# Performance work log

Hardware: AMD Instinct MI355X
Metric: run time of the kernel (lower is better)

The kernel has to match this reference:

```python
import jax, jax.numpy as jnp
import numpy as np

TEMPERATURE = 0.1
NUM_RISK_GROUPS = 4
SIM_WEIGHT = 1.0
CONTRAST_WEIGHT = 0.1
NEG = jnp.float32(-1e9)  # finite stand-in for -inf (grad-safe, exp() == 0 in fp32)


def setup_inputs() -> dict:
    key = jax.random.key(0)
    k1, k2, k3, k4 = jax.random.split(key, 4)
    N, D = 8192, 256
    return {
        "log_risks": jax.random.normal(k1, (N,), dtype=jnp.float32),
        "times": jax.random.uniform(k2, (N,), dtype=jnp.float32),
        "censor": jnp.ones((N,), dtype=jnp.int32),
        "wsi_embeddings": jax.random.normal(k3, (N, D), dtype=jnp.float32),
        "omic_embeddings": jax.random.normal(k4, (N, D), dtype=jnp.float32),
    }


def _cox_loss(log_risks, times, censor):
    lr = jnp.clip(log_risks, -10.0, 10.0)
    order = jnp.argsort(-times)  # descending times
    slr = lr[order]
    sc = censor[order]
    # at-risk sum for index i is sum_{j<=i} exp(slr_j) (arange <= i mask) -> cumsum
    at_risk = jnp.cumsum(jnp.exp(slr))
    li = slr - jnp.log(at_risk + 1e-15)
    mask = (sc == 1)
    cnt = jnp.maximum(jnp.sum(mask), 1)
    return -jnp.sum(jnp.where(mask, li, 0.0)) / cnt


def _similarity_loss(a, b):
    na = jnp.maximum(jnp.linalg.norm(a, axis=1), 1e-8)
    nb = jnp.maximum(jnp.linalg.norm(b, axis=1), 1e-8)
    cos = jnp.clip(jnp.sum(a * b, axis=1) / (na * nb), -1.0, 1.0)
    return jnp.mean(1.0 - cos)


def _contrastive_loss(emb, times):
    # NOTE: assumes censor == 1 for all samples (as in setup_inputs), so the
    # uncensored subset is the whole batch and shapes stay static.
    G = NUM_RISK_GROUPS
    q = jnp.quantile(times, jnp.linspace(0.0, 1.0, G + 1))
    # group = #thresholds q[1..G] that t >= ; max bucket clipped to G-1
    groups = jnp.clip(jnp.sum(times[:, None] >= q[None, 1:], axis=1), 0, G - 1)
    z = emb / jnp.maximum(jnp.linalg.norm(emb, axis=1, keepdims=True), 1e-12)
    sim = (z @ z.T) / TEMPERATURE  # [N, N]
    N = emb.shape[0]
    eye = jnp.eye(N, dtype=bool)
    same = groups[:, None] == groups[None, :]
    pos = same & ~eye
    offdiag = ~eye  # pos | neg == all off-diagonal entries
    lse_pos = jax.nn.logsumexp(jnp.where(pos, sim, NEG), axis=1)
    lse_all = jax.nn.logsumexp(jnp.where(offdiag, sim, NEG), axis=1)
    neg_any = jnp.any(~same & ~eye, axis=1)
    valid = jnp.any(pos, axis=1) & neg_any
    loss = -lse_pos + lse_all
    cnt = jnp.maximum(jnp.sum(valid), 1)
    return jnp.sum(jnp.where(valid, loss, 0.0)) / cnt


def reference(log_risks, times, censor, wsi_embeddings, omic_embeddings):
    cox = _cox_loss(log_risks, times, censor)
    sim = _similarity_loss(wsi_embeddings, omic_embeddings)
    c_wsi = _contrastive_loss(wsi_embeddings, times)
    c_omic = _contrastive_loss(omic_embeddings, times)
    contrast = (c_wsi + c_omic) / 2.0
    return cox + SIM_WEIGHT * sim + CONTRAST_WEIGHT * contrast
```

## Files before the change

### kernel.cpp

```cpp
#include <hip/hip_runtime.h>


#define NN 8192
#define DD 256

typedef __attribute__((ext_vector_type(4))) float f32x4;
typedef __attribute__((ext_vector_type(4))) int i32x4;
typedef __attribute__((ext_vector_type(8))) int i32x8;

__device__ inline void gl_lds16(const void* g, void* l) {
  __builtin_amdgcn_global_load_lds(
      (const __attribute__((address_space(1))) unsigned int*)g,
      (__attribute__((address_space(3))) unsigned int*)l, 16, 0, 0);
}

__global__ void __launch_bounds__(256) k_rows(
    const float* __restrict__ lr, const float* __restrict__ times,
    const int* __restrict__ censor,
    const float* __restrict__ wsi, const float* __restrict__ omic,
    unsigned char* __restrict__ pw, unsigned char* __restrict__ po,
    float* __restrict__ pslots, float* __restrict__ gsum) {
  __shared__ __align__(16) float st[1024];
  __shared__ __align__(16) float se[1024];
  __shared__ float red[4][3];
  const int tid = threadIdx.x;
  const int lane = tid & 63;
  const int wv = tid >> 6;
  const int i = blockIdx.x * 4 + wv;

  if (blockIdx.x < 64) {
    ((f32x4*)gsum)[blockIdx.x * 256 + tid] = (f32x4){0.f, 0.f, 0.f, 0.f};
  }

  const float4 w = ((const float4*)(wsi + (size_t)i * DD))[lane];
  const float4 o = ((const float4*)(omic + (size_t)i * DD))[lane];
  float nw = w.x * w.x + w.y * w.y + w.z * w.z + w.w * w.w;
  float no = o.x * o.x + o.y * o.y + o.z * o.z + o.w * o.w;
  float dd = w.x * o.x + w.y * o.y + w.z * o.z + w.w * o.w;
  for (int m = 1; m < 64; m <<= 1) {
    nw += __shfl_xor(nw, m);
    no += __shfl_xor(no, m);
    dd += __shfl_xor(dd, m);
  }
  const float nws = sqrtf(nw), nos = sqrtf(no);

  const float ti = times[i];
  int rk = 0;
  float ar = 0.f;
  for (int c = 0; c < 8; ++c) {
    __syncthreads();
    for (int p = tid; p < 1024; p += 256) {
      float t = times[c * 1024 + p];
      float l = lr[c * 1024 + p];
      st[p] = t;
      se[p] = __expf(fminf(fmaxf(l, -10.f), 10.f));
    }
    __syncthreads();
#pragma unroll 4
    for (int jt = 0; jt < 16; ++jt) {
      const int p = jt * 64 + lane;
      const float t = st[p];
      const float e = se[p];
      const bool c1 = (t < ti) || ((t == ti) && ((c * 1024 + p) < i));
      rk += c1 ? 1 : 0;
      ar += c1 ? 0.f : e;
    }
  }
  for (int m = 1; m < 64; m <<= 1) {
    rk += __shfl_xor(rk, m);
    ar += __shfl_xor(ar, m);
  }

  if (lane == 0) {
    float c = dd / (fmaxf(nws, 1e-8f) * fmaxf(nos, 1e-8f));
    c = fminf(fmaxf(c, -1.f), 1.f);
    float l = fminf(fmaxf(lr[i], -10.f), 10.f);
    float li = l - logf(ar + 1e-15f);
    bool cen = (censor[i] == 1);
    red[wv][0] = cen ? li : 0.f;
    red[wv][1] = cen ? 1.f : 0.f;
    red[wv][2] = 1.f - c;
  }

  const int r = rk;
  const float iw = 1.f / fmaxf(nws, 1e-12f);
  const float io = 1.f / fmaxf(nos, 1e-12f);
  int zw = __builtin_amdgcn_cvt_pk_fp8_f32(w.x * iw, w.y * iw, 0, false);
  zw = __builtin_amdgcn_cvt_pk_fp8_f32(w.z * iw, w.w * iw, zw, true);
  int zo = __builtin_amdgcn_cvt_pk_fp8_f32(o.x * io, o.y * io, 0, false);
  zo = __builtin_amdgcn_cvt_pk_fp8_f32(o.z * io, o.w * io, zo, true);
  const size_t off = ((size_t)((lane >> 5) * 4 + ((lane >> 3) & 3)) * NN + r) * 32
                     + (lane & 7) * 4;
  *(unsigned int*)(pw + off) = (unsigned int)zw;
  *(unsigned int*)(po + off) = (unsigned int)zo;
  __syncthreads();
  if (tid < 3) {
    pslots[blockIdx.x * 4 + tid] =
        red[0][tid] + red[1][tid] + red[2][tid] + red[3][tid];
  }
}

__global__ void __launch_bounds__(256, 4) k_contrast(
    const unsigned char* __restrict__ pw, const unsigned char* __restrict__ po,
    float* __restrict__ gsum) {
  __shared__ __align__(16) unsigned char sbuf[2][16384];
  const int tid = threadIdx.x;
  const int lane = tid & 63;
  const int wv = tid >> 6;
  const int lo = lane & 15, q = lane >> 4;
  const int cb = blockIdx.x, rb = blockIdx.y, mz = blockIdx.z;
  const unsigned char* __restrict__ pk = (mz == 0) ? pw : po;
  const int rowbase = rb * 128 + wv * 32;
  const int colstart = cb * 512;
  const int g = cb >> 2;

  i32x8 afrag[2][2];
#pragma unroll
  for (int rt = 0; rt < 2; ++rt) {
    const size_t row = rowbase + rt * 16 + lo;
#pragma unroll
    for (int ks = 0; ks < 2; ++ks)
      afrag[rt][ks] = *(const i32x8*)(pk + ((size_t)(ks * 4 + q) * NN + row) * 32);
  }

  const unsigned char* gsrc[4];
#pragma unroll
  for (int p = 0; p < 4; ++p) {
    const int u = (wv * 4 + p) * 64 + lane;
    const int uct = u >> 8, uks = (u >> 7) & 1, uh = (u >> 6) & 1;
    const int ul = u & 63;
    gsrc[p] = pk + ((size_t)(uks * 4 + (ul >> 4)) * NN
                    + colstart + uct * 16 + (ul & 15)) * 32 + uh * 16;
  }
  unsigned char* const ldb = &sbuf[0][(size_t)wv * 4096];

#pragma unroll
  for (int p = 0; p < 4; ++p) gl_lds16(gsrc[p], ldb + p * 1024);
  __syncthreads();

  float s[2][4] = {{0.f}};
  const int dctbase = (wv & 1) * 2;

#pragma unroll 1
  for (int st = 0; st < 8; ++st) {
    if (st < 7) {
      const size_t adv = (size_t)(st + 1) * 2048;
      const size_t bofs = ((st + 1) & 1) ? 16384 : 0;
#pragma unroll
      for (int p = 0; p < 4; ++p) gl_lds16(gsrc[p] + adv, ldb + bofs + p * 1024);
    }
    const unsigned char* buf = &sbuf[st & 1][0];
    const bool diagw = ((rowbase >> 6) == ((colstart + st * 64) >> 6));
#pragma unroll
    for (int ct = 0; ct < 4; ++ct) {
      f32x4 a0 = {0.f, 0.f, 0.f, 0.f}, a1 = {0.f, 0.f, 0.f, 0.f};
#pragma unroll
      for (int ks = 0; ks < 2; ++ks) {
        const int rbase = ((ct * 2 + ks) * 2) * 1024 + lane * 16;
        i32x4 blo = *(const i32x4*)&buf[rbase];
        i32x4 bhi = *(const i32x4*)&buf[rbase + 1024];
        i32x8 b = __builtin_shufflevector(blo, bhi, 0, 1, 2, 3, 4, 5, 6, 7);
        a0 = __builtin_amdgcn_mfma_scale_f32_16x16x128_f8f6f4(
            afrag[0][ks], b, a0, 0, 0, 0, 0x7F, 0, 0x7F);
        a1 = __builtin_amdgcn_mfma_scale_f32_16x16x128_f8f6f4(
            afrag[1][ks], b, a1, 0, 0, 0, 0x7F, 0, 0x7F);
      }
      if (diagw) {
#pragma unroll
        for (int r = 0; r < 4; ++r) {
          float e0 = __builtin_amdgcn_exp2f(fmaf(a0[r], 14.4269504f, -14.4269504f));
          float e1 = __builtin_amdgcn_exp2f(fmaf(a1[r], 14.4269504f, -14.4269504f));
          if (ct == dctbase + 0 && lo == q * 4 + r) e0 = 0.f;
          if (ct == dctbase + 1 && lo == q * 4 + r) e1 = 0.f;
          s[0][r] += e0;
          s[1][r] += e1;
        }
      } else {
#pragma unroll
        for (int r = 0; r < 4; ++r) {
          s[0][r] += __builtin_amdgcn_exp2f(fmaf(a0[r], 14.4269504f, -14.4269504f));
          s[1][r] += __builtin_amdgcn_exp2f(fmaf(a1[r], 14.4269504f, -14.4269504f));
        }
      }
    }
    __syncthreads();
  }

#pragma unroll
  for (int rt = 0; rt < 2; ++rt)
#pragma unroll
    for (int r = 0; r < 4; ++r) {
      float v = s[rt][r];
      v += __shfl_xor(v, 1); v += __shfl_xor(v, 2);
      v += __shfl_xor(v, 4); v += __shfl_xor(v, 8);
      if (lo == 0) {
        const int row = rowbase + rt * 16 + q * 4 + r;
        atomicAdd(&gsum[((size_t)mz * NN + row) * 4 + g], v);
      }
    }
}

__global__ void __launch_bounds__(1024) k_finale(
    const float* __restrict__ pslots, const float* __restrict__ gsum,
    float* __restrict__ out) {
  __shared__ float rsum[16][4];
  const int tid = threadIdx.x;
  const int lane = tid & 63, wv = tid >> 6;
  float cox = 0.f, cnt = 0.f, sim = 0.f, con = 0.f;
  for (int b = tid; b < 2048; b += 1024) {
    const float4 v = ((const float4*)pslots)[b];
    cox += v.x; cnt += v.y; sim += v.z;
  }
  for (int idx = tid; idx < 2 * NN; idx += 1024) {
    const float4 v = ((const float4*)gsum)[idx];
    const int row = idx & (NN - 1);
    const int gg = row >> 11;
    const float sg = (gg == 0) ? v.x : (gg == 1) ? v.y : (gg == 2) ? v.z : v.w;
    con += logf(v.x + v.y + v.z + v.w) - logf(sg);
  }
  for (int m = 1; m < 64; m <<= 1) {
    cox += __shfl_xor(cox, m);
    cnt += __shfl_xor(cnt, m);
    sim += __shfl_xor(sim, m);
    con += __shfl_xor(con, m);
  }
  if (lane == 0) {
    rsum[wv][0] = cox; rsum[wv][1] = cnt; rsum[wv][2] = sim; rsum[wv][3] = con;
  }
  __syncthreads();
  if (tid == 0) {
    float c0 = 0.f, c1 = 0.f, c2 = 0.f, c3 = 0.f;
    for (int k = 0; k < 16; ++k) {
      c0 += rsum[k][0]; c1 += rsum[k][1]; c2 += rsum[k][2]; c3 += rsum[k][3];
    }
    out[0] = -c0 / fmaxf(c1, 1.f) + c2 / (float)NN
             + 0.1f * 0.5f * c3 / (float)NN;
  }
}

extern "C" void kernel_launch(void* const* d_in, const int* in_sizes, int n_in,
                              void* d_out, int out_size, void* d_ws, size_t ws_size,
                              hipStream_t stream) {
  const float* lr = (const float*)d_in[0];
  const float* times = (const float*)d_in[1];
  const int* censor = (const int*)d_in[2];
  const float* wsi = (const float*)d_in[3];
  const float* omic = (const float*)d_in[4];
  float* out = (float*)d_out;

  char* ws = (char*)d_ws;
  float* pslots = (float*)ws;
  float* gsum = (float*)(ws + 32768);
  unsigned char* pw = (unsigned char*)(ws + 294912);
  unsigned char* po = (unsigned char*)(ws + 294912 + 2097152);

  k_rows<<<2048, 256, 0, stream>>>(lr, times, censor, wsi, omic, pw, po, pslots, gsum);
  k_contrast<<<dim3(16, 64, 2), 256, 0, stream>>>(pw, po, gsum);
  k_finale<<<1, 1024, 0, stream>>>(pslots, gsum, out);
}
```

Baseline: 149.1 us.

## Exploit similarity symmetry with triangular tiles and batch four rows per wave

The contrastive kernel now launches only the upper-triangular block tiles of the symmetric N×N similarity matrix. Off-diagonal tiles also accumulate column sums into the per-group totals through atomics, which roughly halves the MFMA and exp work. The temperature/log2 scale is folded into the fp8-normalised embeddings, and the max-offset subtraction is dropped. The rows kernel handles four rows per wave with vectorised LDS reads, amortising the O(N) rank and at-risk scan; the cost is many extra column atomics and a larger score range fed to exp2.

```diff
diff --git a/kernel.cpp b/kernel.cpp
--- a/kernel.cpp
+++ b/kernel.cpp
@@ -3,6 +3,7 @@
 
 #define NN 8192
 #define DD 256
+#define SCL 3.7982826f
 
 typedef __attribute__((ext_vector_type(4))) float f32x4;
 typedef __attribute__((ext_vector_type(4))) int i32x4;
@@ -26,73 +27,102 @@
   const int tid = threadIdx.x;
   const int lane = tid & 63;
   const int wv = tid >> 6;
-  const int i = blockIdx.x * 4 + wv;
+  const int i0 = blockIdx.x * 16 + wv * 4;
 
   if (blockIdx.x < 64) {
     ((f32x4*)gsum)[blockIdx.x * 256 + tid] = (f32x4){0.f, 0.f, 0.f, 0.f};
   }
 
-  const float4 w = ((const float4*)(wsi + (size_t)i * DD))[lane];
-  const float4 o = ((const float4*)(omic + (size_t)i * DD))[lane];
-  float nw = w.x * w.x + w.y * w.y + w.z * w.z + w.w * w.w;
-  float no = o.x * o.x + o.y * o.y + o.z * o.z + o.w * o.w;
-  float dd = w.x * o.x + w.y * o.y + w.z * o.z + w.w * o.w;
-  for (int m = 1; m < 64; m <<= 1) {
-    nw += __shfl_xor(nw, m);
-    no += __shfl_xor(no, m);
-    dd += __shfl_xor(dd, m);
-  }
-  const float nws = sqrtf(nw), nos = sqrtf(no);
-
-  const float ti = times[i];
-  int rk = 0;
-  float ar = 0.f;
+  float ti[4];
+#pragma unroll
+  for (int rr = 0; rr < 4; ++rr) ti[rr] = times[i0 + rr];
+
+  int rk[4] = {0, 0, 0, 0};
+  float ar[4] = {0.f, 0.f, 0.f, 0.f};
   for (int c = 0; c < 8; ++c) {
     __syncthreads();
-    for (int p = tid; p < 1024; p += 256) {
-      float t = times[c * 1024 + p];
-      float l = lr[c * 1024 + p];
-      st[p] = t;
-      se[p] = __expf(fminf(fmaxf(l, -10.f), 10.f));
+    {
+      const float4 t4 = ((const float4*)(times + c * 1024))[tid];
+      const float4 l4 = ((const float4*)(lr + c * 1024))[tid];
+      ((float4*)st)[tid] = t4;
+      float4 e4;
+      e4.x = __expf(fminf(fmaxf(l4.x, -10.f), 10.f));
+      e4.y = __expf(fminf(fmaxf(l4.y, -10.f), 10.f));
+      e4.z = __expf(fminf(fmaxf(l4.z, -10.f), 10.f));
+      e4.w = __expf(fminf(fmaxf(l4.w, -10.f), 10.f));
+      ((float4*)se)[tid] = e4;
     }
     __syncthreads();
-#pragma unroll 4
-    for (int jt = 0; jt < 16; ++jt) {
+#pragma unroll
+    for (int jt = 0; jt < 4; ++jt) {
       const int p = jt * 64 + lane;
-      const float t = st[p];
-      const float e = se[p];
-      const bool c1 = (t < ti) || ((t == ti) && ((c * 1024 + p) < i));
-      rk += c1 ? 1 : 0;
-      ar += c1 ? 0.f : e;
-    }
-  }
+      const float4 t = ((const float4*)st)[p];
+      const float4 e = ((const float4*)se)[p];
+      const int jb = c * 1024 + p * 4;
+#define UPD(TV, EV, JJ)                                                  \
+  {                                                                      \
+    _Pragma("unroll") for (int rr = 0; rr < 4; ++rr) {                   \
+      const bool c1 = ((TV) < ti[rr]) ||                                 \
+                      (((TV) == ti[rr]) && ((JJ) < i0 + rr));            \
+      rk[rr] += c1 ? 1 : 0;                                              \
+      ar[rr] += c1 ? 0.f : (EV);                                         \
+    }                                                                    \
+  }
+      UPD(t.x, e.x, jb + 0)
+      UPD(t.y, e.y, jb + 1)
+      UPD(t.z, e.z, jb + 2)
+      UPD(t.w, e.w, jb + 3)
+#undef UPD
+    }
+  }
+#pragma unroll
   for (int m = 1; m < 64; m <<= 1) {
-    rk += __shfl_xor(rk, m);
-    ar += __shfl_xor(ar, m);
-  }
-
+#pragma unroll
+    for (int rr = 0; rr < 4; ++rr) {
+      rk[rr] += __shfl_xor(rk[rr], m);
+      ar[rr] += __shfl_xor(ar[rr], m);
+    }
+  }
+
+  float scox = 0.f, scnt = 0.f, ssim = 0.f;
+#pragma unroll
+  for (int rr = 0; rr < 4; ++rr) {
+    const int i = i0 + rr;
+    const float4 w = ((const float4*)(wsi + (size_t)i * DD))[lane];
+    const float4 o = ((const float4*)(omic + (size_t)i * DD))[lane];
+    float nw = w.x * w.x + w.y * w.y + w.z * w.z + w.w * w.w;
+    float no = o.x * o.x + o.y * o.y + o.z * o.z + o.w * o.w;
+    float dd = w.x * o.x + w.y * o.y + w.z * o.z + w.w * o.w;
+#pragma unroll
+    for (int m = 1; m < 64; m <<= 1) {
+      nw += __shfl_xor(nw, m);
+      no += __shfl_xor(no, m);
+      dd += __shfl_xor(dd, m);
+    }
+    const float nws = sqrtf(nw), nos = sqrtf(no);
+    if (lane == 0) {
+      float cc = dd / (fmaxf(nws, 1e-8f) * fmaxf(nos, 1e-8f));
+      cc = fminf(fmaxf(cc, -1.f), 1.f);
+      const float l = fminf(fmaxf(lr[i], -10.f), 10.f);
+      const float li = l - logf(ar[rr] + 1e-15f);
+      if (censor[i] == 1) { scox += li; scnt += 1.f; }
+      ssim += 1.f - cc;
+    }
+    const float iw = SCL / fmaxf(nws, 1e-12f);
+    const float io = SCL / fmaxf(nos, 1e-12f);
+    int zw = __builtin_amdgcn_cvt_pk_fp8_f32(w.x * iw, w.y * iw, 0, false);
+    zw = __builtin_amdgcn_cvt_pk_fp8_f32(w.z * iw, w.w * iw, zw, true);
+    int zo = __builtin_amdgcn_cvt_pk_fp8_f32(o.x * io, o.y * io, 0, false);
+    zo = __builtin_amdgcn_cvt_pk_fp8_f32(o.z * io, o.w * io, zo, true);
+    const size_t off =
+        ((size_t)((lane >> 5) * 4 + ((lane >> 3) & 3)) * NN + rk[rr]) * 32 +
+        (lane & 7) * 4;
+    *(unsigned int*)(pw + off) = (unsigned int)zw;
+    *(unsigned int*)(po + off) = (unsigned int)zo;
+  }
   if (lane == 0) {
-    float c = dd / (fmaxf(nws, 1e-8f) * fmaxf(nos, 1e-8f));
-    c = fminf(fmaxf(c, -1.f), 1.f);
-    float l = fminf(fmaxf(lr[i], -10.f), 10.f);
-    float li = l - logf(ar + 1e-15f);
-    bool cen = (censor[i] == 1);
-    red[wv][0] = cen ? li : 0.f;
-    red[wv][1] = cen ? 1.f : 0.f;
-    red[wv][2] = 1.f - c;
-  }
-
-  const int r = rk;
-  const float iw = 1.f / fmaxf(nws, 1e-12f);
-  const float io = 1.f / fmaxf(nos, 1e-12f);
-  int zw = __builtin_amdgcn_cvt_pk_fp8_f32(w.x * iw, w.y * iw, 0, false);
-  zw = __builtin_amdgcn_cvt_pk_fp8_f32(w.z * iw, w.w * iw, zw, true);
-  int zo = __builtin_amdgcn_cvt_pk_fp8_f32(o.x * io, o.y * io, 0, false);
-  zo = __builtin_amdgcn_cvt_pk_fp8_f32(o.z * io, o.w * io, zo, true);
-  const size_t off = ((size_t)((lane >> 5) * 4 + ((lane >> 3) & 3)) * NN + r) * 32
-                     + (lane & 7) * 4;
-  *(unsigned int*)(pw + off) = (unsigned int)zw;
-  *(unsigned int*)(po + off) = (unsigned int)zo;
+    red[wv][0] = scox; red[wv][1] = scnt; red[wv][2] = ssim;
+  }
   __syncthreads();
   if (tid < 3) {
     pslots[blockIdx.x * 4 + tid] =
@@ -108,11 +138,20 @@
   const int lane = tid & 63;
   const int wv = tid >> 6;
   const int lo = lane & 15, q = lane >> 4;
-  const int cb = blockIdx.x, rb = blockIdx.y, mz = blockIdx.z;
+  const int mz = blockIdx.z;
   const unsigned char* __restrict__ pk = (mz == 0) ? pw : po;
+
+  const int tt = blockIdx.x;
+  int cb = (int)((sqrtf((float)(2 * tt + 1)) - 1.f) * 0.5f);
+  while (2 * (cb + 1) * (cb + 2) <= tt) ++cb;
+  while (cb > 0 && 2 * cb * (cb + 1) > tt) --cb;
+  const int rb = tt - 2 * cb * (cb + 1);
+  const bool isUpper = rb < 4 * cb;
+
   const int rowbase = rb * 128 + wv * 32;
-  const int colstart = cb * 512;
+  const int colstart = cb * 512 + blockIdx.y * 256;
   const int g = cb >> 2;
+  const int grow = rb >> 4;
 
   i32x8 afrag[2][2];
 #pragma unroll
@@ -142,8 +181,8 @@
   const int dctbase = (wv & 1) * 2;
 
 #pragma unroll 1
-  for (int st = 0; st < 8; ++st) {
-    if (st < 7) {
+  for (int st = 0; st < 4; ++st) {
+    if (st < 3) {
       const size_t adv = (size_t)(st + 1) * 2048;
       const size_t bofs = ((st + 1) & 1) ? 16384 : 0;
 #pragma unroll
@@ -165,11 +204,12 @@
         a1 = __builtin_amdgcn_mfma_scale_f32_16x16x128_f8f6f4(
             afrag[1][ks], b, a1, 0, 0, 0, 0x7F, 0, 0x7F);
       }
+      float csum = 0.f;
       if (diagw) {
 #pragma unroll
         for (int r = 0; r < 4; ++r) {
-          float e0 = __builtin_amdgcn_exp2f(fmaf(a0[r], 14.4269504f, -14.4269504f));
-          float e1 = __builtin_amdgcn_exp2f(fmaf(a1[r], 14.4269504f, -14.4269504f));
+          float e0 = __builtin_amdgcn_exp2f(a0[r]);
+          float e1 = __builtin_amdgcn_exp2f(a1[r]);
           if (ct == dctbase + 0 && lo == q * 4 + r) e0 = 0.f;
           if (ct == dctbase + 1 && lo == q * 4 + r) e1 = 0.f;
           s[0][r] += e0;
@@ -178,8 +218,19 @@
       } else {
 #pragma unroll
         for (int r = 0; r < 4; ++r) {
-          s[0][r] += __builtin_amdgcn_exp2f(fmaf(a0[r], 14.4269504f, -14.4269504f));
-          s[1][r] += __builtin_amdgcn_exp2f(fmaf(a1[r], 14.4269504f, -14.4269504f));
+          const float e0 = __builtin_amdgcn_exp2f(a0[r]);
+          const float e1 = __builtin_amdgcn_exp2f(a1[r]);
+          s[0][r] += e0;
+          s[1][r] += e1;
+          csum += e0 + e1;
+        }
+      }
+      if (isUpper) {
+        csum += __shfl_xor(csum, 16);
+        csum += __shfl_xor(csum, 32);
+        if (lane < 16) {
+          const int col = colstart + st * 64 + ct * 16 + lane;
+          atomicAdd(&gsum[((size_t)mz * NN + col) * 4 + grow], csum);
         }
       }
     }
@@ -207,7 +258,7 @@
   const int tid = threadIdx.x;
   const int lane = tid & 63, wv = tid >> 6;
   float cox = 0.f, cnt = 0.f, sim = 0.f, con = 0.f;
-  for (int b = tid; b < 2048; b += 1024) {
+  for (int b = tid; b < 512; b += 1024) {
     const float4 v = ((const float4*)pslots)[b];
     cox += v.x; cnt += v.y; sim += v.z;
   }
@@ -254,7 +305,7 @@
   unsigned char* pw = (unsigned char*)(ws + 294912);
   unsigned char* po = (unsigned char*)(ws + 294912 + 2097152);
 
-  k_rows<<<2048, 256, 0, stream>>>(lr, times, censor, wsi, omic, pw, po, pslots, gsum);
-  k_contrast<<<dim3(16, 64, 2), 256, 0, stream>>>(pw, po, gsum);
+  k_rows<<<512, 256, 0, stream>>>(lr, times, censor, wsi, omic, pw, po, pslots, gsum);
+  k_contrast<<<dim3(544, 2, 2), 256, 0, stream>>>(pw, po, gsum);
   k_finale<<<1, 1024, 0, stream>>>(pslots, gsum, out);
 }
```

Result: slower. 184.0 us (+23.4%).
